# Kernel optimization log

Hardware: AMD Instinct MI355X
Metric: run time of the kernel (lower is better)

Reference implementation:

```python
import jax, jax.numpy as jnp
import numpy as np

B, T, C = 2, 2048, 1024
N_HEAD = 16
HEAD_DIM = C // N_HEAD


def setup_inputs() -> dict:
    key = jax.random.key(0)
    k1, k2, k3 = jax.random.split(key, 3)
    x = jax.random.normal(k1, (B, T, C), dtype=jnp.float32)
    # broadcastable causal mask: 1 where attendable, 0 where masked
    mask = jnp.tril(jnp.ones((T, T), dtype=jnp.int32))[None, None, :, :]
    W_qkv = jax.random.normal(k2, (C, 3 * C), dtype=jnp.float32) * (1.0 / np.sqrt(C))
    b_qkv = jnp.zeros((3 * C,), dtype=jnp.float32)
    W_out = jax.random.normal(k3, (C, C), dtype=jnp.float32) * (1.0 / np.sqrt(C))
    b_out = jnp.zeros((C,), dtype=jnp.float32)
    return {"x": x, "mask": mask, "W_qkv": W_qkv, "b_qkv": b_qkv, "W_out": W_out, "b_out": b_out}


def reference(x, mask, W_qkv, b_qkv, W_out, b_out):
    Bx, Tx, Cx = x.shape
    # fused QKV projection
    qkv = x @ W_qkv + b_qkv  # [B, T, 3C]
    qkv = qkv.reshape(Bx, Tx, 3, N_HEAD, HEAD_DIM).transpose(2, 0, 3, 1, 4)  # [3, B, H, T, D]
    q, k, v = qkv[0], qkv[1], qkv[2]
    scale = 1.0 / jnp.sqrt(jnp.asarray(HEAD_DIM, dtype=x.dtype))
    att = jnp.einsum('bhqd,bhkd->bhqk', q, k) * scale  # [B, H, T, T]
    att = jnp.where(mask == 0, -jnp.inf, att)
    att = jax.nn.softmax(att, axis=-1)
    # dropout is deterministic=True in the original -> identity
    y = jnp.einsum('bhqk,bhkd->bhqd', att, v)  # [B, H, T, D]
    y = y.transpose(0, 2, 1, 3).reshape(Bx, Tx, Cx)
    return y @ W_out + b_out
```

## Files before the change

kernel.cpp:

```cpp
#include <hip/hip_runtime.h>
#include <hip/hip_bf16.h>
#include <math.h>

#define B_  2
#define T_  2048
#define C_  1024
#define NH  16
#define HD  64

typedef __attribute__((ext_vector_type(8))) short short8;
typedef __attribute__((ext_vector_type(4))) float f32x4;

__device__ __forceinline__ void gload_lds16(const void* g, void* l) {
    __builtin_amdgcn_global_load_lds(
        (const __attribute__((address_space(1))) void*)g,
        (__attribute__((address_space(3))) void*)l, 16, 0, 0);
}

__device__ __forceinline__ unsigned short f2bf(float f) {
    __hip_bfloat16 b = __float2bfloat16(f);
    return *reinterpret_cast<unsigned short*>(&b);
}

__global__ __launch_bounds__(256) void cast_bf16_kernel(
    const float* __restrict__ in, __hip_bfloat16* __restrict__ out, int n4)
{
    const int i = blockIdx.x * 256 + threadIdx.x;
    if (i >= n4) return;
    const float4 v = reinterpret_cast<const float4*>(in)[i];
    ushort4 o;
    o.x = f2bf(v.x); o.y = f2bf(v.y); o.z = f2bf(v.z); o.w = f2bf(v.w);
    reinterpret_cast<ushort4*>(out)[i] = o;
}

__global__ __launch_bounds__(256) void transpose_cast_kernel(
    const float* __restrict__ W, __hip_bfloat16* __restrict__ Wt, int R, int Ccols)
{
    __shared__ float tile[32][33];
    const int c0 = blockIdx.x * 32, r0 = blockIdx.y * 32;
    const int tx = threadIdx.x & 31, ty = threadIdx.x >> 5;
    #pragma unroll
    for (int i = 0; i < 32; i += 8)
        tile[ty + i][tx] = W[(size_t)(r0 + ty + i) * Ccols + c0 + tx];
    __syncthreads();
    #pragma unroll
    for (int i = 0; i < 32; i += 8)
        Wt[(size_t)(c0 + ty + i) * R + r0 + tx] = __float2bfloat16(tile[tx][ty + i]);
}

#define GBM 128
#define GBN 128
#define GBK 64

__global__ __launch_bounds__(256) void gemm_bf16_mfma(
    const __hip_bfloat16* __restrict__ A,
    const __hip_bfloat16* __restrict__ Bt,
    const float* __restrict__ bias,
    float* __restrict__ Cf,
    __hip_bfloat16* __restrict__ Cb,
    __hip_bfloat16* __restrict__ vt,
    int M, int N, int K, int gx)
{
    __shared__ __align__(16) __hip_bfloat16 As[GBM * GBK];
    __shared__ __align__(16) __hip_bfloat16 Bs[GBN * GBK];

    const int nwg = (int)gridDim.x;
    const int orig = (int)blockIdx.x;
    const int qq = nwg >> 3, rr = nwg & 7;
    const int xcd = orig & 7, off = orig >> 3;
    const int wgid = (xcd < rr ? xcd * (qq + 1)
                               : rr * (qq + 1) + (xcd - rr) * qq) + off;
    const int bx = wgid % gx;
    const int by = wgid / gx;

    const int tid = threadIdx.x;
    const int lane = tid & 63;
    const int wid = tid >> 6;
    const int wr = wid >> 1, wc = wid & 1;
    const int lr = lane & 15;
    const int lk = (lane >> 4) * 8;

    const size_t rowA0 = (size_t)by * GBM;
    const size_t colB0 = (size_t)bx * GBN;

    f32x4 acc[4][4];
    #pragma unroll
    for (int i = 0; i < 4; ++i)
        #pragma unroll
        for (int j = 0; j < 4; ++j)
            acc[i][j] = (f32x4){0.f, 0.f, 0.f, 0.f};

    for (int k0 = 0; k0 < K; k0 += GBK) {
        #pragma unroll
        for (int it = 0; it < 4; ++it) {
            const int idx = tid + it * 256;
            const int r  = idx >> 3;
            const int kc = (idx & 7) * 8;
            gload_lds16(A  + (rowA0 + r) * K + k0 + kc, &As[idx * 8]);
            gload_lds16(Bt + (colB0 + r) * K + k0 + kc, &Bs[idx * 8]);
        }
        __syncthreads();

        #pragma unroll
        for (int kk = 0; kk < GBK; kk += 32) {
            short8 af[4], bf[4];
            #pragma unroll
            for (int i = 0; i < 4; ++i)
                af[i] = *reinterpret_cast<const short8*>(
                    &As[(wr * 64 + i * 16 + lr) * GBK + kk + lk]);
            #pragma unroll
            for (int j = 0; j < 4; ++j)
                bf[j] = *reinterpret_cast<const short8*>(
                    &Bs[(wc * 64 + j * 16 + lr) * GBK + kk + lk]);
            #pragma unroll
            for (int i = 0; i < 4; ++i)
                #pragma unroll
                for (int j = 0; j < 4; ++j)
                    acc[i][j] = __builtin_amdgcn_mfma_f32_16x16x32_bf16(
                        af[i], bf[j], acc[i][j], 0, 0, 0);
        }
        __syncthreads();
    }

    const int orow = (lane >> 4) * 4;
    #pragma unroll
    for (int i = 0; i < 4; ++i) {
        #pragma unroll
        for (int j = 0; j < 4; ++j) {
            const size_t col = colB0 + wc * 64 + j * 16 + lr;
            const float bb = bias[col];
            float v[4];
            #pragma unroll
            for (int r = 0; r < 4; ++r) v[r] = acc[i][j][r] + bb;
            const size_t row0 = rowA0 + wr * 64 + i * 16 + orow;
            if (Cf) {
                #pragma unroll
                for (int r = 0; r < 4; ++r)
                    Cf[(row0 + r) * N + col] = v[r];
            } else {
                #pragma unroll
                for (int r = 0; r < 4; ++r)
                    Cb[(row0 + r) * N + col] = __float2bfloat16(v[r]);
            }
            if (vt && (int)col >= 2 * C_) {
                const int vc = (int)col - 2 * C_;
                const int hh = vc >> 6, dd = vc & 63;
                const int bb_ = (int)(row0 >> 11);
                const int t0  = (int)(row0 & 2047);
                ushort4 o;
                o.x = f2bf(v[0]); o.y = f2bf(v[1]); o.z = f2bf(v[2]); o.w = f2bf(v[3]);
                *reinterpret_cast<ushort4*>(
                    vt + (((size_t)(bb_ * NH + hh) * 64 + dd) * T_ + t0)) = o;
            }
        }
    }
}

__global__ __launch_bounds__(256) void attn_mfma_kernel(
    const __hip_bfloat16* __restrict__ qkvb,
    const __hip_bfloat16* __restrict__ vtg,
    __hip_bfloat16* __restrict__ yb)
{
    const int bh = blockIdx.x;
    const int b = bh >> 4, h = bh & 15;
    const int qt = (int)gridDim.y - 1 - (int)blockIdx.y;
    const int tid = threadIdx.x;
    const int w = tid >> 6, lane = tid & 63;
    const int lr = lane & 15, lg = lane >> 4;

    __shared__ __align__(16) __hip_bfloat16 Ks[2][64 * 64];
    __shared__ __align__(16) __hip_bfloat16 Vts[2][64 * 64];
    __shared__ __align__(16) __hip_bfloat16 Pl[4][16 * 64];

    const int qrow = qt * 64 + w * 16;
    const size_t s3C = 3 * C_;

    const float qscale = 0.125f * 1.44269504f;
    const __hip_bfloat16* qp =
        qkvb + ((size_t)(b * T_) + qrow + lr) * s3C + h * 64 + lg * 8;
    short8 qf0 = *reinterpret_cast<const short8*>(qp);
    short8 qf1 = *reinterpret_cast<const short8*>(qp + 32);
    #pragma unroll
    for (int j = 0; j < 8; ++j) {
        const float f0 = __uint_as_float(((unsigned)(unsigned short)qf0[j]) << 16);
        const float f1 = __uint_as_float(((unsigned)(unsigned short)qf1[j]) << 16);
        qf0[j] = (short)f2bf(f0 * qscale);
        qf1[j] = (short)f2bf(f1 * qscale);
    }

    short8 vone;
    #pragma unroll
    for (int j = 0; j < 8; ++j) vone[j] = (lr == 0) ? (short)0x3F80 : (short)0;

    f32x4 o_acc[5];
    #pragma unroll
    for (int db = 0; db < 5; ++db) o_acc[db] = (f32x4){0.f, 0.f, 0.f, 0.f};

    char* PlB = (char*)Pl[w];

    auto STAGE = [&](int t, int bi) {
        #pragma unroll
        for (int rr = 0; rr < 2; ++rr) {
            const int slot = (rr * 4 + w) * 64 + lane;
            const int row = slot >> 3;
            const int gblk = (slot & 7) ^ (row & 7);
            gload_lds16(qkvb + ((size_t)(b * T_) + t * 64 + row) * s3C
                             + C_ + h * 64 + gblk * 8,
                        (char*)Ks[bi] + slot * 16);
            gload_lds16(vtg + ((size_t)bh * 64 + row) * T_ + t * 64 + gblk * 8,
                        (char*)Vts[bi] + slot * 16);
        }
    };

    STAGE(0, 0);
    __syncthreads();
    int buf = 0;

    for (int t = 0; t <= qt; ++t) {
        if (t < qt) STAGE(t + 1, buf ^ 1);

        const char* KsB  = (const char*)Ks[buf];
        const char* VtsB = (const char*)Vts[buf];

        f32x4 sacc[4];
        #pragma unroll
        for (int kb = 0; kb < 4; ++kb) sacc[kb] = (f32x4){0.f, 0.f, 0.f, 0.f};
        __builtin_amdgcn_s_setprio(1);
        #pragma unroll
        for (int kb = 0; kb < 4; ++kb) {
            const int key = kb * 16 + lr;
            const short8 kf0 = *reinterpret_cast<const short8*>(
                KsB + key * 128 + ((lg) ^ (key & 7)) * 16);
            const short8 kf1 = *reinterpret_cast<const short8*>(
                KsB + key * 128 + ((4 + lg) ^ (key & 7)) * 16);
            sacc[kb] = __builtin_amdgcn_mfma_f32_16x16x32_bf16(qf0, kf0, sacc[kb], 0, 0, 0);
            sacc[kb] = __builtin_amdgcn_mfma_f32_16x16x32_bf16(qf1, kf1, sacc[kb], 0, 0, 0);
        }
        __builtin_amdgcn_s_setprio(0);

        const bool diag = (t == qt);
        #pragma unroll
        for (int r = 0; r < 4; ++r) {
            const int qlocal = lg * 4 + r;
            #pragma unroll
            for (int kb = 0; kb < 4; ++kb) {
                float s = sacc[kb][r];
                if (diag) {
                    const int keyg = t * 64 + kb * 16 + lr;
                    s = (keyg <= qrow + qlocal) ? s : -INFINITY;
                }
                const float p = exp2f(s);
                const int key = kb * 16 + lr;
                const int byte = qlocal * 128
                               + (((key >> 3) ^ (qlocal & 7)) * 16) + (key & 7) * 2;
                *reinterpret_cast<__hip_bfloat16*>(PlB + byte) = __float2bfloat16(p);
            }
        }

        const short8 pf0 = *reinterpret_cast<const short8*>(
            PlB + lr * 128 + ((lg) ^ (lr & 7)) * 16);
        const short8 pf1 = *reinterpret_cast<const short8*>(
            PlB + lr * 128 + ((4 + lg) ^ (lr & 7)) * 16);
        __builtin_amdgcn_s_setprio(1);
        #pragma unroll
        for (int db = 0; db < 4; ++db) {
            const int dd = db * 16 + lr;
            const short8 vf0 = *reinterpret_cast<const short8*>(
                VtsB + dd * 128 + ((lg) ^ (dd & 7)) * 16);
            const short8 vf1 = *reinterpret_cast<const short8*>(
                VtsB + dd * 128 + ((4 + lg) ^ (dd & 7)) * 16);
            o_acc[db] = __builtin_amdgcn_mfma_f32_16x16x32_bf16(pf0, vf0, o_acc[db], 0, 0, 0);
            o_acc[db] = __builtin_amdgcn_mfma_f32_16x16x32_bf16(pf1, vf1, o_acc[db], 0, 0, 0);
        }
        o_acc[4] = __builtin_amdgcn_mfma_f32_16x16x32_bf16(pf0, vone, o_acc[4], 0, 0, 0);
        o_acc[4] = __builtin_amdgcn_mfma_f32_16x16x32_bf16(pf1, vone, o_acc[4], 0, 0, 0);
        __builtin_amdgcn_s_setprio(0);

        __syncthreads();
        buf ^= 1;
    }

    #pragma unroll
    for (int r = 0; r < 4; ++r) {
        const float lsum = __shfl(o_acc[4][r], (lane & 48));
        const float inv = 1.f / lsum;
        const int qg = qrow + lg * 4 + r;
        __hip_bfloat16* yp = yb + ((size_t)(b * T_) + qg) * C_ + h * 64;
        #pragma unroll
        for (int db = 0; db < 4; ++db)
            yp[db * 16 + lr] = __float2bfloat16(o_acc[db][r] * inv);
    }
}

extern "C" void kernel_launch(void* const* d_in, const int* in_sizes, int n_in,
                              void* d_out, int out_size, void* d_ws, size_t ws_size,
                              hipStream_t stream)
{
    const float* x     = (const float*)d_in[0];
    const float* W_qkv = (const float*)d_in[2];
    const float* b_qkv = (const float*)d_in[3];
    const float* W_out = (const float*)d_in[4];
    const float* b_out = (const float*)d_in[5];
    float* out = (float*)d_out;

    __hip_bfloat16* qkvb = (__hip_bfloat16*)d_ws;
    __hip_bfloat16* vtg  = qkvb + (size_t)B_ * T_ * 3 * C_;
    __hip_bfloat16* xb   = vtg  + (size_t)B_ * NH * 64 * T_;
    __hip_bfloat16* wqt  = xb   + (size_t)B_ * T_ * C_;
    __hip_bfloat16* wot  = wqt  + (size_t)3 * C_ * C_;
    __hip_bfloat16* yb   = wot  + (size_t)C_ * C_;

    const int M = B_ * T_;

    cast_bf16_kernel<<<(M * C_ / 4 + 255) / 256, 256, 0, stream>>>(x, xb, M * C_ / 4);
    {
        dim3 g(3 * C_ / 32, C_ / 32);
        transpose_cast_kernel<<<g, 256, 0, stream>>>(W_qkv, wqt, C_, 3 * C_);
    }
    {
        dim3 g(C_ / 32, C_ / 32);
        transpose_cast_kernel<<<g, 256, 0, stream>>>(W_out, wot, C_, C_);
    }

    {
        const int gx = 3 * C_ / GBN, gy = M / GBM;
        gemm_bf16_mfma<<<dim3(gx * gy), 256, 0, stream>>>(
            xb, wqt, b_qkv, nullptr, qkvb, vtg, M, 3 * C_, C_, gx);
    }
    {
        dim3 grid(B_ * NH, T_ / 64);
        attn_mfma_kernel<<<grid, 256, 0, stream>>>(qkvb, vtg, yb);
    }
    {
        const int gx = C_ / GBN, gy = M / GBM;
        gemm_bf16_mfma<<<dim3(gx * gy), 256, 0, stream>>>(
            yb, wot, b_out, out, nullptr, nullptr, M, C_, C_, gx);
    }
}
```

Before: 222.9 us.

## Use 256x256 multi-stage pipelined GEMM with swizzled LDS for QKV projection

```diff
diff --git a/kernel.cpp b/kernel.cpp
--- a/kernel.cpp
+++ b/kernel.cpp
@@ -48,21 +48,20 @@
         Wt[(size_t)(c0 + ty + i) * R + r0 + tx] = __float2bfloat16(tile[tx][ty + i]);
 }
 
-#define GBM 128
-#define GBN 128
-#define GBK 64
-
-__global__ __launch_bounds__(256) void gemm_bf16_mfma(
+#define QBM 256
+#define QBN 256
+#define QBK 32
+
+__global__ __launch_bounds__(512) void gemm_bf16_8ph(
     const __hip_bfloat16* __restrict__ A,
     const __hip_bfloat16* __restrict__ Bt,
     const float* __restrict__ bias,
-    float* __restrict__ Cf,
     __hip_bfloat16* __restrict__ Cb,
     __hip_bfloat16* __restrict__ vt,
     int M, int N, int K, int gx)
 {
-    __shared__ __align__(16) __hip_bfloat16 As[GBM * GBK];
-    __shared__ __align__(16) __hip_bfloat16 Bs[GBN * GBK];
+    __shared__ __align__(16) __hip_bfloat16 As[4][QBM * QBK];
+    __shared__ __align__(16) __hip_bfloat16 Bs[4][QBN * QBK];
 
     const int nwg = (int)gridDim.x;
     const int orig = (int)blockIdx.x;
@@ -74,74 +73,103 @@
     const int by = wgid / gx;
 
     const int tid = threadIdx.x;
-    const int lane = tid & 63;
-    const int wid = tid >> 6;
-    const int wr = wid >> 1, wc = wid & 1;
-    const int lr = lane & 15;
-    const int lk = (lane >> 4) * 8;
-
-    const size_t rowA0 = (size_t)by * GBM;
-    const size_t colB0 = (size_t)bx * GBN;
-
-    f32x4 acc[4][4];
-    #pragma unroll
-    for (int i = 0; i < 4; ++i)
+    const int w = tid >> 6, lane = tid & 63;
+    const int wm = w >> 2, wn = w & 3;
+    const int lr = lane & 15, kb = lane >> 4;
+
+    const size_t rowA0 = (size_t)by * QBM;
+    const size_t colB0 = (size_t)bx * QBN;
+
+    const int rS   = tid >> 2;
+    const int blkl = tid & 3;
+    const int bsw  = blkl ^ ((rS >> 1) & 3);
+    const __hip_bfloat16* gA0 = A  + (rowA0 + rS) * K + bsw * 8;
+    const __hip_bfloat16* gA1 = gA0 + (size_t)128 * K;
+    const __hip_bfloat16* gB0 = Bt + (colB0 + rS) * K + bsw * 8;
+    const __hip_bfloat16* gB1 = gB0 + (size_t)128 * K;
+
+    const int NT = K / QBK;
+
+    #define STAGE_A(t) { char* d = (char*)As[(t) & 3] + tid * 16;            \
+        gload_lds16(gA0 + (t) * QBK, d);                                     \
+        gload_lds16(gA1 + (t) * QBK, d + 8192); }
+    #define STAGE_B(t) { char* d = (char*)Bs[(t) & 3] + tid * 16;            \
+        gload_lds16(gB0 + (t) * QBK, d);                                     \
+        gload_lds16(gB1 + (t) * QBK, d + 8192); }
+
+    const int rowAl = wm * 128 + lr;
+    const int rowBl = wn * 64 + lr;
+    const int ofsA = rowAl * 64 + (kb ^ ((rowAl >> 1) & 3)) * 16;
+    const int ofsB = rowBl * 64 + (kb ^ ((rowBl >> 1) & 3)) * 16;
+
+    f32x4 acc[8][4];
+    #pragma unroll
+    for (int i = 0; i < 8; ++i)
         #pragma unroll
         for (int j = 0; j < 4; ++j)
             acc[i][j] = (f32x4){0.f, 0.f, 0.f, 0.f};
 
-    for (int k0 = 0; k0 < K; k0 += GBK) {
-        #pragma unroll
-        for (int it = 0; it < 4; ++it) {
-            const int idx = tid + it * 256;
-            const int r  = idx >> 3;
-            const int kc = (idx & 7) * 8;
-            gload_lds16(A  + (rowA0 + r) * K + k0 + kc, &As[idx * 8]);
-            gload_lds16(Bt + (colB0 + r) * K + k0 + kc, &Bs[idx * 8]);
-        }
-        __syncthreads();
-
-        #pragma unroll
-        for (int kk = 0; kk < GBK; kk += 32) {
-            short8 af[4], bf[4];
-            #pragma unroll
-            for (int i = 0; i < 4; ++i)
-                af[i] = *reinterpret_cast<const short8*>(
-                    &As[(wr * 64 + i * 16 + lr) * GBK + kk + lk]);
+    STAGE_A(0); STAGE_B(0);
+    STAGE_A(1); STAGE_B(1);
+    STAGE_A(2); STAGE_B(2);
+
+    for (int t = 0; t < NT; ++t) {
+        if (t + 2 < NT)      asm volatile("s_waitcnt vmcnt(8)" ::: "memory");
+        else if (t + 1 < NT) asm volatile("s_waitcnt vmcnt(4)" ::: "memory");
+        else                 asm volatile("s_waitcnt vmcnt(0)" ::: "memory");
+        __builtin_amdgcn_s_barrier();
+        __builtin_amdgcn_sched_barrier(0);
+
+        const char* Ab = (const char*)As[t & 3];
+        const char* Bb = (const char*)Bs[t & 3];
+
+        short8 bf[4], af[4];
+        #pragma unroll
+        for (int j = 0; j < 4; ++j)
+            bf[j] = *reinterpret_cast<const short8*>(Bb + ofsB + 1024 * j);
+        #pragma unroll
+        for (int i = 0; i < 4; ++i)
+            af[i] = *reinterpret_cast<const short8*>(Ab + ofsA + 1024 * i);
+        if (t + 3 < NT) STAGE_A(t + 3);
+        __builtin_amdgcn_s_setprio(1);
+        #pragma unroll
+        for (int i = 0; i < 4; ++i)
             #pragma unroll
             for (int j = 0; j < 4; ++j)
-                bf[j] = *reinterpret_cast<const short8*>(
-                    &Bs[(wc * 64 + j * 16 + lr) * GBK + kk + lk]);
-            #pragma unroll
-            for (int i = 0; i < 4; ++i)
-                #pragma unroll
-                for (int j = 0; j < 4; ++j)
-                    acc[i][j] = __builtin_amdgcn_mfma_f32_16x16x32_bf16(
-                        af[i], bf[j], acc[i][j], 0, 0, 0);
-        }
-        __syncthreads();
-    }
-
-    const int orow = (lane >> 4) * 4;
-    #pragma unroll
-    for (int i = 0; i < 4; ++i) {
+                acc[i][j] = __builtin_amdgcn_mfma_f32_16x16x32_bf16(
+                    af[i], bf[j], acc[i][j], 0, 0, 0);
+        __builtin_amdgcn_s_setprio(0);
+
+        __builtin_amdgcn_s_barrier();
+        __builtin_amdgcn_sched_barrier(0);
+        #pragma unroll
+        for (int i = 0; i < 4; ++i)
+            af[i] = *reinterpret_cast<const short8*>(Ab + ofsA + 1024 * (i + 4));
+        if (t + 3 < NT) STAGE_B(t + 3);
+        __builtin_amdgcn_s_setprio(1);
+        #pragma unroll
+        for (int i = 0; i < 4; ++i)
+            #pragma unroll
+            for (int j = 0; j < 4; ++j)
+                acc[i + 4][j] = __builtin_amdgcn_mfma_f32_16x16x32_bf16(
+                    af[i], bf[j], acc[i + 4][j], 0, 0, 0);
+        __builtin_amdgcn_s_setprio(0);
+    }
+
+    const int orow4 = (lane >> 4) * 4;
+    #pragma unroll
+    for (int i = 0; i < 8; ++i) {
         #pragma unroll
         for (int j = 0; j < 4; ++j) {
-            const size_t col = colB0 + wc * 64 + j * 16 + lr;
+            const size_t col = colB0 + wn * 64 + j * 16 + lr;
             const float bb = bias[col];
             float v[4];
             #pragma unroll
             for (int r = 0; r < 4; ++r) v[r] = acc[i][j][r] + bb;
-            const size_t row0 = rowA0 + wr * 64 + i * 16 + orow;
-            if (Cf) {
-                #pragma unroll
-                for (int r = 0; r < 4; ++r)
-                    Cf[(row0 + r) * N + col] = v[r];
-            } else {
-                #pragma unroll
-                for (int r = 0; r < 4; ++r)
-                    Cb[(row0 + r) * N + col] = __float2bfloat16(v[r]);
-            }
+            const size_t row0 = rowA0 + wm * 128 + i * 16 + orow4;
+            #pragma unroll
+            for (int r = 0; r < 4; ++r)
+                Cb[(row0 + r) * N + col] = __float2bfloat16(v[r]);
             if (vt && (int)col >= 2 * C_) {
                 const int vc = (int)col - 2 * C_;
                 const int hh = vc >> 6, dd = vc & 63;
@@ -151,6 +179,96 @@
                 o.x = f2bf(v[0]); o.y = f2bf(v[1]); o.z = f2bf(v[2]); o.w = f2bf(v[3]);
                 *reinterpret_cast<ushort4*>(
                     vt + (((size_t)(bb_ * NH + hh) * 64 + dd) * T_ + t0)) = o;
+            }
+        }
+    }
+    #undef STAGE_A
+    #undef STAGE_B
+}
+
+#define GBM 128
+#define GBN 128
+#define GBK 64
+
+__global__ __launch_bounds__(256) void gemm_bf16_mfma(
+    const __hip_bfloat16* __restrict__ A,
+    const __hip_bfloat16* __restrict__ Bt,
+    const float* __restrict__ bias,
+    float* __restrict__ Cf,
+    int M, int N, int K, int gx)
+{
+    __shared__ __align__(16) __hip_bfloat16 As[GBM * GBK];
+    __shared__ __align__(16) __hip_bfloat16 Bs[GBN * GBK];
+
+    const int nwg = (int)gridDim.x;
+    const int orig = (int)blockIdx.x;
+    const int qq = nwg >> 3, rr = nwg & 7;
+    const int xcd = orig & 7, off = orig >> 3;
+    const int wgid = (xcd < rr ? xcd * (qq + 1)
+                               : rr * (qq + 1) + (xcd - rr) * qq) + off;
+    const int bx = wgid % gx;
+    const int by = wgid / gx;
+
+    const int tid = threadIdx.x;
+    const int lane = tid & 63;
+    const int wid = tid >> 6;
+    const int wr = wid >> 1, wc = wid & 1;
+    const int lr = lane & 15;
+    const int lk = (lane >> 4) * 8;
+
+    const size_t rowA0 = (size_t)by * GBM;
+    const size_t colB0 = (size_t)bx * GBN;
+
+    f32x4 acc[4][4];
+    #pragma unroll
+    for (int i = 0; i < 4; ++i)
+        #pragma unroll
+        for (int j = 0; j < 4; ++j)
+            acc[i][j] = (f32x4){0.f, 0.f, 0.f, 0.f};
+
+    for (int k0 = 0; k0 < K; k0 += GBK) {
+        #pragma unroll
+        for (int it = 0; it < 4; ++it) {
+            const int idx = tid + it * 256;
+            const int r  = idx >> 3;
+            const int kc = (idx & 7) * 8;
+            gload_lds16(A  + (rowA0 + r) * K + k0 + kc, &As[idx * 8]);
+            gload_lds16(Bt + (colB0 + r) * K + k0 + kc, &Bs[idx * 8]);
+        }
+        __syncthreads();
+
+        #pragma unroll
+        for (int kk = 0; kk < GBK; kk += 32) {
+            short8 af[4], bf[4];
+            #pragma unroll
+            for (int i = 0; i < 4; ++i)
+                af[i] = *reinterpret_cast<const short8*>(
+                    &As[(wr * 64 + i * 16 + lr) * GBK + kk + lk]);
+            #pragma unroll
+            for (int j = 0; j < 4; ++j)
+                bf[j] = *reinterpret_cast<const short8*>(
+                    &Bs[(wc * 64 + j * 16 + lr) * GBK + kk + lk]);
+            #pragma unroll
+            for (int i = 0; i < 4; ++i)
+                #pragma unroll
+                for (int j = 0; j < 4; ++j)
+                    acc[i][j] = __builtin_amdgcn_mfma_f32_16x16x32_bf16(
+                        af[i], bf[j], acc[i][j], 0, 0, 0);
+        }
+        __syncthreads();
+    }
+
+    const int orow = (lane >> 4) * 4;
+    #pragma unroll
+    for (int i = 0; i < 4; ++i) {
+        #pragma unroll
+        for (int j = 0; j < 4; ++j) {
+            const size_t col = colB0 + wc * 64 + j * 16 + lr;
+            const float bb = bias[col];
+            #pragma unroll
+            for (int r = 0; r < 4; ++r) {
+                const size_t row = rowA0 + wr * 64 + i * 16 + orow + r;
+                Cf[row * N + col] = acc[i][j][r] + bb;
             }
         }
     }
@@ -323,9 +441,9 @@
     }
 
     {
-        const int gx = 3 * C_ / GBN, gy = M / GBM;
-        gemm_bf16_mfma<<<dim3(gx * gy), 256, 0, stream>>>(
-            xb, wqt, b_qkv, nullptr, qkvb, vtg, M, 3 * C_, C_, gx);
+        const int gx = 3 * C_ / QBN, gy = M / QBM;
+        gemm_bf16_8ph<<<dim3(gx * gy), 512, 0, stream>>>(
+            xb, wqt, b_qkv, qkvb, vtg, M, 3 * C_, C_, gx);
     }
     {
         dim3 grid(B_ * NH, T_ / 64);
@@ -334,6 +452,6 @@
     {
         const int gx = C_ / GBN, gy = M / GBM;
         gemm_bf16_mfma<<<dim3(gx * gy), 256, 0, stream>>>(
-            yb, wot, b_out, out, nullptr, nullptr, M, C_, C_, gx);
-    }
-}
+            yb, wot, b_out, out, M, C_, C_, gx);
+    }
+}
```

After: 203.9 us. 8.5% less time.
